# Kernel tuning notes

Measured on AMD Instinct MI355X. Metric: run time of the kernel, lower is better.

Reference implementation:

```python
import jax, jax.numpy as jnp
import numpy as np

# 22-joint tree (parents[i] < i); feet at 18, 21; spine at 2 (stand-in for get_totalcapture_skeleton)
PARENTS = [-1, 0, 1, 2, 3, 4, 3, 6, 7, 8, 3, 10, 11, 12, 1, 14, 15, 16, 17, 1, 19, 20]
FEET = [18, 21]
SPINE = 2
LAMBDAS = dict(root=5.0, rot=1.0, pos=2.0, vel=1.0, smooth=0.5, contact=2.0, floor=2.0, tilt=1.0)


def _normalize(x, eps=1e-12):
    return x / jnp.maximum(jnp.linalg.norm(x, axis=-1, keepdims=True), eps)


def cont6d_to_mat(d6):
    # d6: (..., 6) -> (..., 3, 3) with columns (b1, b2, b3)
    a1, a2 = d6[..., :3], d6[..., 3:]
    b1 = _normalize(a1)
    b2 = _normalize(a2 - b1 * jnp.sum(b1 * a2, axis=-1, keepdims=True))
    b3 = jnp.cross(b1, b2)
    return jnp.stack((b1, b2, b3), axis=-1)


def run_canonical_fk(full_output, offsets):
    # full_output: (B, S, 22, 6); root forced to identity rot / zero pos
    B, S, J, _ = full_output.shape
    rot_mats = cont6d_to_mat(full_output)  # (B, S, 22, 3, 3)
    eye = jnp.broadcast_to(jnp.eye(3, dtype=full_output.dtype), (B, S, 3, 3))
    zeros = jnp.zeros((B, S, 3), dtype=full_output.dtype)
    g_rots = [None] * J
    g_pos = [None] * J
    g_rots[0], g_pos[0] = eye, zeros
    for i in range(1, J):
        p = PARENTS[i]
        g_rots[i] = jnp.einsum('bsij,bsjk->bsik', g_rots[p], rot_mats[:, :, i])
        g_pos[i] = g_pos[p] + jnp.einsum('bsij,j->bsi', g_rots[p], offsets[i])
    return jnp.stack(g_pos, axis=2)  # (B, S, 22, 3)


def mse(a, b):
    return jnp.mean(jnp.square(a - b))


def motion_loss(pred_full, target_full, offsets):
    l_root = mse(pred_full[:, :, 0, :3], target_full[:, :, 0, :3]) + \
             mse(pred_full[:, :, 1, :], target_full[:, :, 1, :])
    l_rot = mse(pred_full[:, :, 2:], target_full[:, :, 2:])

    pred_pos = run_canonical_fk(pred_full, offsets)
    gt_pos = run_canonical_fk(target_full, offsets)
    l_pos = mse(pred_pos, gt_pos)

    pred_vel = pred_pos[:, 1:] - pred_pos[:, :-1]
    gt_vel = gt_pos[:, 1:] - gt_pos[:, :-1]
    l_vel = mse(pred_vel, gt_vel)

    pred_acc = pred_vel[:, 1:] - pred_vel[:, :-1]
    gt_acc = gt_vel[:, 1:] - gt_vel[:, :-1]
    l_smooth = mse(pred_acc, gt_acc)

    feet = jnp.array(FEET)
    l_floor = mse(pred_pos[:, :, feet, 1], gt_pos[:, :, feet, 1])

    gt_feet_vel = gt_vel[:, :, feet, :]
    pred_feet_vel = pred_vel[:, :, feet, :]
    is_planted = (jnp.linalg.norm(gt_feet_vel, axis=-1) < 0.005).astype(pred_full.dtype)
    l_contact = jnp.mean(jnp.linalg.norm(pred_feet_vel, axis=-1) * is_planted)

    pred_spine = cont6d_to_mat(pred_full[:, :, SPINE])
    gt_spine = cont6d_to_mat(target_full[:, :, SPINE])
    # R @ [0,1,0]^T == second column of R
    l_tilt = mse(pred_spine[..., :, 1], gt_spine[..., :, 1])

    total = (LAMBDAS['root'] * l_root + LAMBDAS['rot'] * l_rot + LAMBDAS['pos'] * l_pos +
             LAMBDAS['vel'] * l_vel + LAMBDAS['smooth'] * l_smooth + LAMBDAS['contact'] * l_contact +
             LAMBDAS['floor'] * l_floor + LAMBDAS['tilt'] * l_tilt)
    return total


def setup_inputs() -> dict:
    key = jax.random.key(0)
    k1, k2 = jax.random.split(key)
    B, S, J, C = 256, 512, 22, 6
    pred_full = jax.random.normal(k1, (B, S, J, C), dtype=jnp.float32)
    target_full = jax.random.normal(k2, (B, S, J, C), dtype=jnp.float32)
    rng = np.random.default_rng(42)
    off = rng.normal(size=(J, 3)).astype(np.float32) * 0.1
    off[0] = 0.0
    offsets = jnp.asarray(off)
    return {"pred_full": pred_full, "target_full": target_full, "offsets": offsets}


def reference(pred_full, target_full, offsets):
    return motion_loss(pred_full, target_full, offsets)
```

## Files before the change

### kernel.cpp

```cpp
#include <hip/hip_runtime.h>

namespace {

constexpr int kB = 256;
constexpr int kS = 512;
constexpr int CHUNK  = 62;
constexpr int NCHUNK = (kS + CHUNK - 1) / CHUNK;
constexpr int NSLOT  = 64;
constexpr int LDSF   = 2304;

constexpr float BSf   = 131072.f;
constexpr float K_R1  = 5.0f / (BSf * 3.f);
constexpr float K_R2  = 5.0f / (BSf * 6.f);
constexpr float K_ROT = 1.0f / (BSf * 120.f);
constexpr float K_POS = 2.0f / (BSf * 66.f);
constexpr float K_VEL = 1.0f / (256.f * 511.f * 66.f);
constexpr float K_SMO = 0.5f / (256.f * 510.f * 66.f);
constexpr float K_FLO = 2.0f / (BSf * 2.f);
constexpr float K_CON = 2.0f / (256.f * 511.f * 2.f);
constexpr float K_TIL = 1.0f / (BSf * 3.f);

__device__ __forceinline__ void cont6d(const float a[6], float R[3][3]) {
    float n1 = a[0]*a[0] + a[1]*a[1] + a[2]*a[2];
    float i1 = __frsqrt_rn(fmaxf(n1, 1e-24f));
    float b1x = a[0]*i1, b1y = a[1]*i1, b1z = a[2]*i1;
    float dp  = b1x*a[3] + b1y*a[4] + b1z*a[5];
    float ux = a[3] - b1x*dp, uy = a[4] - b1y*dp, uz = a[5] - b1z*dp;
    float n2 = ux*ux + uy*uy + uz*uz;
    float i2 = __frsqrt_rn(fmaxf(n2, 1e-24f));
    float b2x = ux*i2, b2y = uy*i2, b2z = uz*i2;
    R[0][0] = b1x; R[1][0] = b1y; R[2][0] = b1z;
    R[0][1] = b2x; R[1][1] = b2y; R[2][1] = b2z;
    R[0][2] = b1y*b2z - b1z*b2y;
    R[1][2] = b1z*b2x - b1x*b2z;
    R[2][2] = b1x*b2y - b1y*b2x;
}

template<int C2, int FB>
__device__ __forceinline__ void stage(const float* __restrict__ pred,
                                      const float* __restrict__ targ,
                                      size_t rowbase, int s0,
                                      float* __restrict__ ldsw, int lane) {
    constexpr int V = 64 * C2;
    constexpr int R = (2 * V) / 64;
    const float* pp_ = pred + rowbase * 132 + FB;
    const float* tp_ = targ + rowbase * 132 + FB;
    float2 st[18];
    #pragma unroll
    for (int r = 0; r < R; ++r) {
        int u = r * 64 + lane;
        int t2 = (u >= V) ? 1 : 0;
        int uu = u - t2 * V;
        int f = uu / C2;
        int c = uu - f * C2;
        int sf = s0 + f; sf = (sf < kS) ? sf : (kS - 1);
        const float* bp = t2 ? tp_ : pp_;
        st[r] = *reinterpret_cast<const float2*>(bp + (size_t)sf * 132 + 2 * c);
    }
    float2* l2 = reinterpret_cast<float2*>(ldsw);
    #pragma unroll
    for (int r = 0; r < R; ++r)
        l2[r * 64 + lane] = st[r];
}

__device__ __forceinline__ void read6f(const float2* __restrict__ b, int jj, float a[6]) {
    float2 x = b[jj*3], y = b[jj*3+1], z = b[jj*3+2];
    a[0]=x.x; a[1]=x.y; a[2]=y.x; a[3]=y.y; a[4]=z.x; a[5]=z.y;
}

template<bool NEED_R, bool SPINE_J, bool FOOT>
__device__ __forceinline__ void joint_step(
    const float aP[6], const float aT[6], const float* __restrict__ off,
    const float RpP[3][3], const float ppP[3], float RnP[3][3], float pnP[3],
    const float RpT[3][3], const float ppT[3], float RnT[3][3], float pnT[3],
    float wf, float wv, float wa, float& s)
{
    float dsum = 0.f;
    #pragma unroll
    for (int k = 0; k < 6; ++k) { float dd = aP[k] - aT[k]; dsum += dd*dd; }
    s += wf * (K_ROT * dsum);

    const float ox = off[0], oy = off[1], oz = off[2];
    #pragma unroll
    for (int r = 0; r < 3; ++r) {
        pnP[r] = ppP[r] + RpP[r][0]*ox + RpP[r][1]*oy + RpP[r][2]*oz;
        pnT[r] = ppT[r] + RpT[r][0]*ox + RpT[r][1]*oy + RpT[r][2]*oz;
    }

    if constexpr (NEED_R) {
        float RlP[3][3], RlT[3][3];
        cont6d(aP, RlP);
        cont6d(aT, RlT);
        if constexpr (SPINE_J) {
            float t0 = RlP[0][1] - RlT[0][1];
            float t1 = RlP[1][1] - RlT[1][1];
            float t2 = RlP[2][1] - RlT[2][1];
            s += wf * (K_TIL * (t0*t0 + t1*t1 + t2*t2));
        }
        #pragma unroll
        for (int r = 0; r < 3; ++r)
            #pragma unroll
            for (int c = 0; c < 3; ++c) {
                RnP[r][c] = RpP[r][0]*RlP[0][c] + RpP[r][1]*RlP[1][c] + RpP[r][2]*RlP[2][c];
                RnT[r][c] = RpT[r][0]*RlT[0][c] + RpT[r][1]*RlT[1][c] + RpT[r][2]*RlT[2][c];
            }
    }

    float d[3], d1[3];
    #pragma unroll
    for (int r = 0; r < 3; ++r) d[r] = pnP[r] - pnT[r];
    s += wf * (K_POS * (d[0]*d[0] + d[1]*d[1] + d[2]*d[2]));

    float va = 0.f, sa = 0.f;
    #pragma unroll
    for (int r = 0; r < 3; ++r) {
        d1[r]    = __shfl_down(d[r], 1);
        float d2 = __shfl_down(d[r], 2);
        float dv = d1[r] - d[r];            va += dv*dv;
        float ds = d2 - 2.f*d1[r] + d[r];   sa += ds*ds;
    }
    s += wv * (K_VEL * va);
    s += wa * (K_SMO * sa);

    if constexpr (FOOT) {
        s += wf * (K_FLO * (d[1]*d[1]));
        float gx = __shfl_down(pnT[0], 1) - pnT[0];
        float gy = __shfl_down(pnT[1], 1) - pnT[1];
        float gz = __shfl_down(pnT[2], 1) - pnT[2];
        float pvx = gx + (d1[0] - d[0]);
        float pvy = gy + (d1[1] - d[1]);
        float pvz = gz + (d1[2] - d[2]);
        float planted = (gx*gx + gy*gy + gz*gz < 2.5e-5f) ? 1.f : 0.f;
        s += wv * (K_CON * (planted * sqrtf(pvx*pvx + pvy*pvy + pvz*pvz)));
    }
}

__global__ __launch_bounds__(64)
void motion_loss_kernel(const float* __restrict__ pred,
                        const float* __restrict__ targ,
                        const float* __restrict__ offs,
                        float* __restrict__ acc)
{
    __shared__ float lds[LDSF];

    const int lane = threadIdx.x;
    const int cg    = blockIdx.x;
    const int b     = cg / NCHUNK;
    const int chunk = cg - b * NCHUNK;
    const int s0    = chunk * CHUNK;
    const int s     = s0 + lane;
    const size_t rowbase = (size_t)b * kS;

    const float wf = (lane < CHUNK && s     < kS) ? 1.f : 0.f;
    const float wv = (lane < CHUNK && s + 1 < kS) ? 1.f : 0.f;
    const float wa = (lane < CHUNK && s + 2 < kS) ? 1.f : 0.f;

    float2* l2 = reinterpret_cast<float2*>(lds);
    const float2* pb9 = l2 + lane * 9;
    const float2* tb9 = l2 + 576 + lane * 9;

    float loss = 0.f;

    float R1P[3][3], R3P[3][3], RAP[3][3], RBP[3][3];
    float R1T[3][3], R3T[3][3], RAT[3][3], RBT[3][3];
    float p1[3], p3P[3], pAP[3], pBP[3], pSP[3];
    float          p3T[3], pAT[3], pBT[3], pST[3];
    auto& p1P = p1; auto& p1T = p1;

    #define JS(J, JJ, NR, SP, FT, RP, PP, RN, PN) { \
        float aP_[6], aT_[6]; read6f(pb9, JJ, aP_); read6f(tb9, JJ, aT_); \
        joint_step<NR, SP, FT>(aP_, aT_, offs + (J)*3, \
            RP##P, PP##P, RN##P, PN##P, RP##T, PP##T, RN##T, PN##T, \
            wf, wv, wa, loss); }
    #define SB __builtin_amdgcn_sched_barrier(0)

    stage<9, 0>(pred, targ, rowbase, s0, lds, lane);
    {
        float aP_[6], aT_[6];
        read6f(pb9, 0, aP_); read6f(tb9, 0, aT_);
        float d0 = aP_[0]-aT_[0], d1 = aP_[1]-aT_[1], d2 = aP_[2]-aT_[2];
        loss += wf * (K_R1 * (d0*d0 + d1*d1 + d2*d2));
    }
    {
        float aP_[6], aT_[6];
        read6f(pb9, 1, aP_); read6f(tb9, 1, aT_);
        float dsum = 0.f;
        #pragma unroll
        for (int k = 0; k < 6; ++k) { float dd = aP_[k]-aT_[k]; dsum += dd*dd; }
        loss += wf * (K_R2 * dsum);
        cont6d(aP_, R1P);
        cont6d(aT_, R1T);
        p1[0] = offs[3]; p1[1] = offs[4]; p1[2] = offs[5];
    }
    JS( 2, 2, true , true , false, R1, p1, RA, pA);

    SB; stage<9, 18>(pred, targ, rowbase, s0, lds, lane);
    JS( 3, 0, true , false, false, RA, pA, R3, p3);
    JS( 4, 1, true , false, false, R3, p3, RA, pA);
    JS( 5, 2, false, false, false, RA, pA, RB, pS);

    SB; stage<9, 36>(pred, targ, rowbase, s0, lds, lane);
    JS( 6, 0, true , false, false, R3, p3, RA, pA);
    JS( 7, 1, true , false, false, RA, pA, RB, pB);
    JS( 8, 2, true , false, false, RB, pB, RA, pA);

    SB; stage<9, 54>(pred, targ, rowbase, s0, lds, lane);
    JS( 9, 0, false, false, false, RA, pA, RB, pS);
    JS(10, 1, true , false, false, R3, p3, RB, pB);
    JS(11, 2, true , false, false, RB, pB, RA, pA);

    SB; stage<9, 72>(pred, targ, rowbase, s0, lds, lane);
    JS(12, 0, true , false, false, RA, pA, RB, pB);
    JS(13, 1, false, false, false, RB, pB, RA, pS);
    JS(14, 2, true , false, false, R1, p1, RA, pA);

    SB; stage<9, 90>(pred, targ, rowbase, s0, lds, lane);
    JS(15, 0, true , false, false, RA, pA, RB, pB);
    JS(16, 1, true , false, false, RB, pB, RA, pA);
    JS(17, 2, true , false, false, RA, pA, RB, pB);

    SB; stage<9, 108>(pred, targ, rowbase, s0, lds, lane);
    JS(18, 0, false, false, true , RB, pB, RA, pS);
    JS(19, 1, true , false, false, R1, p1, RA, pA);
    JS(20, 2, true , false, false, RA, pA, RB, pB);

    SB; stage<3, 126>(pred, targ, rowbase, s0, lds, lane);
    {
        const float2* pb3 = l2 + lane * 3;
        const float2* tb3 = l2 + 192 + lane * 3;
        float aP_[6], aT_[6];
        read6f(pb3, 0, aP_); read6f(tb3, 0, aT_);
        joint_step<false, false, true>(aP_, aT_, offs + 21*3,
            RBP, pBP, RAP, pSP, RBT, pBT, RAT, pST, wf, wv, wa, loss);
    }
    #undef JS
    #undef SB

    float v = loss;
    #pragma unroll
    for (int o = 32; o > 0; o >>= 1) v += __shfl_xor(v, o);
    if (lane == 0) atomicAdd(&acc[cg & (NSLOT - 1)], v);
}

__global__ void finalize_kernel(const float* __restrict__ acc, float* __restrict__ out) {
    float v = acc[threadIdx.x];
    #pragma unroll
    for (int o = 32; o > 0; o >>= 1) v += __shfl_xor(v, o);
    if (threadIdx.x == 0) out[0] = v;
}

}

extern "C" void kernel_launch(void* const* d_in, const int* in_sizes, int n_in,
                              void* d_out, int out_size, void* d_ws, size_t ws_size,
                              hipStream_t stream) {
    const float* pred = (const float*)d_in[0];
    const float* targ = (const float*)d_in[1];
    const float* offs = (const float*)d_in[2];
    float* acc = (float*)d_ws;

    hipMemsetAsync(acc, 0, NSLOT * sizeof(float), stream);
    motion_loss_kernel<<<dim3(kB * NCHUNK), dim3(64), 0, stream>>>(pred, targ, offs, acc);
    finalize_kernel<<<1, 64, 0, stream>>>(acc, (float*)d_out);
}
```

Before: 64.71 us.

## Triple-buffer global-to-LDS async loads with two joints per stage

Replaces the synchronous register-staged global-to-LDS copies with direct global_load_lds 16-byte asynchronous transfers into three rotating LDS buffers. Each stage now holds two joints (12 floats) for pred and target, and loads for later stages are issued ahead while the current joints are processed, with explicit vmcnt/lgkmcnt waits. This is meant to hide global memory latency behind the FK math in a single-wave block. It raises LDS use and depends on hand-counted wait values and on the single-wave LDS ordering being correct.

New measurement: 62.62 us. -3.2%, faster.

```diff
diff --git a/kernel.cpp b/kernel.cpp
--- a/kernel.cpp
+++ b/kernel.cpp
@@ -5,9 +5,10 @@
 constexpr int kB = 256;
 constexpr int kS = 512;
 constexpr int CHUNK  = 62;
-constexpr int NCHUNK = (kS + CHUNK - 1) / CHUNK;
+constexpr int NCHUNK = 9;
 constexpr int NSLOT  = 64;
-constexpr int LDSF   = 2304;
+constexpr int BUFF   = 1536;
+constexpr int LDSF   = 3 * BUFF;
 
 constexpr float BSf   = 131072.f;
 constexpr float K_R1  = 5.0f / (BSf * 3.f);
@@ -36,38 +37,6 @@
     R[2][2] = b1x*b2y - b1y*b2x;
 }
 
-template<int C2, int FB>
-__device__ __forceinline__ void stage(const float* __restrict__ pred,
-                                      const float* __restrict__ targ,
-                                      size_t rowbase, int s0,
-                                      float* __restrict__ ldsw, int lane) {
-    constexpr int V = 64 * C2;
-    constexpr int R = (2 * V) / 64;
-    const float* pp_ = pred + rowbase * 132 + FB;
-    const float* tp_ = targ + rowbase * 132 + FB;
-    float2 st[18];
-    #pragma unroll
-    for (int r = 0; r < R; ++r) {
-        int u = r * 64 + lane;
-        int t2 = (u >= V) ? 1 : 0;
-        int uu = u - t2 * V;
-        int f = uu / C2;
-        int c = uu - f * C2;
-        int sf = s0 + f; sf = (sf < kS) ? sf : (kS - 1);
-        const float* bp = t2 ? tp_ : pp_;
-        st[r] = *reinterpret_cast<const float2*>(bp + (size_t)sf * 132 + 2 * c);
-    }
-    float2* l2 = reinterpret_cast<float2*>(ldsw);
-    #pragma unroll
-    for (int r = 0; r < R; ++r)
-        l2[r * 64 + lane] = st[r];
-}
-
-__device__ __forceinline__ void read6f(const float2* __restrict__ b, int jj, float a[6]) {
-    float2 x = b[jj*3], y = b[jj*3+1], z = b[jj*3+2];
-    a[0]=x.x; a[1]=x.y; a[2]=y.x; a[3]=y.y; a[4]=z.x; a[5]=z.y;
-}
-
 template<bool NEED_R, bool SPINE_J, bool FOOT>
 __device__ __forceinline__ void joint_step(
     const float aP[6], const float aT[6], const float* __restrict__ off,
@@ -149,92 +118,155 @@
     const int chunk = cg - b * NCHUNK;
     const int s0    = chunk * CHUNK;
     const int s     = s0 + lane;
-    const size_t rowbase = (size_t)b * kS;
 
     const float wf = (lane < CHUNK && s     < kS) ? 1.f : 0.f;
     const float wv = (lane < CHUNK && s + 1 < kS) ? 1.f : 0.f;
     const float wa = (lane < CHUNK && s + 2 < kS) ? 1.f : 0.f;
 
-    float2* l2 = reinterpret_cast<float2*>(lds);
-    const float2* pb9 = l2 + lane * 9;
-    const float2* tb9 = l2 + 576 + lane * 9;
+    const float* predb = pred + (size_t)b * kS * 132;
+    const float* targb = targ + (size_t)b * kS * 132;
+
+    auto issue = [&](int FB, float* buf) {
+        #pragma unroll
+        for (int r = 0; r < 6; ++r) {
+            const float* tb = (r < 3) ? predb : targb;
+            int uu = (r % 3) * 64 + lane;
+            int f  = uu / 3;
+            int c  = uu - f * 3;
+            int sf = s0 + f; sf = (sf < kS) ? sf : (kS - 1);
+            const float* src = tb + (size_t)sf * 132 + FB + 4 * c;
+            __builtin_amdgcn_global_load_lds(
+                (const __attribute__((address_space(1))) void*)src,
+                (__attribute__((address_space(3))) void*)(buf + r * 256),
+                16, 0, 0);
+        }
+    };
+
+    float* buf0 = lds;
+    float* buf1 = lds + BUFF;
+    float* buf2 = lds + 2 * BUFF;
+
+    #define VW(N) do { asm volatile("s_waitcnt vmcnt(" #N ")" ::: "memory"); \
+                       __builtin_amdgcn_sched_barrier(0); } while (0)
+    #define LW0   do { asm volatile("s_waitcnt lgkmcnt(0)" ::: "memory"); \
+                       __builtin_amdgcn_sched_barrier(0); } while (0)
+
+    auto rd6 = [&](const float* base, int jj, float a[6]) {
+        const float2* q = reinterpret_cast<const float2*>(base + jj * 6);
+        float2 x = q[0], y = q[1], z = q[2];
+        a[0]=x.x; a[1]=x.y; a[2]=y.x; a[3]=y.y; a[4]=z.x; a[5]=z.y;
+    };
+
+    issue(0,  buf0);
+    issue(12, buf1);
+    issue(24, buf2);
 
     float loss = 0.f;
-
     float R1P[3][3], R3P[3][3], RAP[3][3], RBP[3][3];
     float R1T[3][3], R3T[3][3], RAT[3][3], RBT[3][3];
     float p1[3], p3P[3], pAP[3], pBP[3], pSP[3];
     float          p3T[3], pAT[3], pBT[3], pST[3];
     auto& p1P = p1; auto& p1T = p1;
 
-    #define JS(J, JJ, NR, SP, FT, RP, PP, RN, PN) { \
-        float aP_[6], aT_[6]; read6f(pb9, JJ, aP_); read6f(tb9, JJ, aT_); \
-        joint_step<NR, SP, FT>(aP_, aT_, offs + (J)*3, \
+    #define RD2(BUF) float aP0[6], aT0[6], aP1[6], aT1[6]; { \
+        const float* pb_ = (BUF) + lane * 12; \
+        const float* tb_ = (BUF) + 768 + lane * 12; \
+        rd6(pb_, 0, aP0); rd6(tb_, 0, aT0); rd6(pb_, 1, aP1); rd6(tb_, 1, aT1); }
+
+    #define JS(AP, AT, J, NR, SP, FT, RP, PP, RN, PN) \
+        joint_step<NR, SP, FT>(AP, AT, offs + (J)*3, \
             RP##P, PP##P, RN##P, PN##P, RP##T, PP##T, RN##T, PN##T, \
-            wf, wv, wa, loss); }
-    #define SB __builtin_amdgcn_sched_barrier(0)
-
-    stage<9, 0>(pred, targ, rowbase, s0, lds, lane);
-    {
-        float aP_[6], aT_[6];
-        read6f(pb9, 0, aP_); read6f(tb9, 0, aT_);
-        float d0 = aP_[0]-aT_[0], d1 = aP_[1]-aT_[1], d2 = aP_[2]-aT_[2];
-        loss += wf * (K_R1 * (d0*d0 + d1*d1 + d2*d2));
-    }
-    {
-        float aP_[6], aT_[6];
-        read6f(pb9, 1, aP_); read6f(tb9, 1, aT_);
-        float dsum = 0.f;
-        #pragma unroll
-        for (int k = 0; k < 6; ++k) { float dd = aP_[k]-aT_[k]; dsum += dd*dd; }
-        loss += wf * (K_R2 * dsum);
-        cont6d(aP_, R1P);
-        cont6d(aT_, R1T);
-        p1[0] = offs[3]; p1[1] = offs[4]; p1[2] = offs[5];
-    }
-    JS( 2, 2, true , true , false, R1, p1, RA, pA);
-
-    SB; stage<9, 18>(pred, targ, rowbase, s0, lds, lane);
-    JS( 3, 0, true , false, false, RA, pA, R3, p3);
-    JS( 4, 1, true , false, false, R3, p3, RA, pA);
-    JS( 5, 2, false, false, false, RA, pA, RB, pS);
-
-    SB; stage<9, 36>(pred, targ, rowbase, s0, lds, lane);
-    JS( 6, 0, true , false, false, R3, p3, RA, pA);
-    JS( 7, 1, true , false, false, RA, pA, RB, pB);
-    JS( 8, 2, true , false, false, RB, pB, RA, pA);
-
-    SB; stage<9, 54>(pred, targ, rowbase, s0, lds, lane);
-    JS( 9, 0, false, false, false, RA, pA, RB, pS);
-    JS(10, 1, true , false, false, R3, p3, RB, pB);
-    JS(11, 2, true , false, false, RB, pB, RA, pA);
-
-    SB; stage<9, 72>(pred, targ, rowbase, s0, lds, lane);
-    JS(12, 0, true , false, false, RA, pA, RB, pB);
-    JS(13, 1, false, false, false, RB, pB, RA, pS);
-    JS(14, 2, true , false, false, R1, p1, RA, pA);
-
-    SB; stage<9, 90>(pred, targ, rowbase, s0, lds, lane);
-    JS(15, 0, true , false, false, RA, pA, RB, pB);
-    JS(16, 1, true , false, false, RB, pB, RA, pA);
-    JS(17, 2, true , false, false, RA, pA, RB, pB);
-
-    SB; stage<9, 108>(pred, targ, rowbase, s0, lds, lane);
-    JS(18, 0, false, false, true , RB, pB, RA, pS);
-    JS(19, 1, true , false, false, R1, p1, RA, pA);
-    JS(20, 2, true , false, false, RA, pA, RB, pB);
-
-    SB; stage<3, 126>(pred, targ, rowbase, s0, lds, lane);
-    {
-        const float2* pb3 = l2 + lane * 3;
-        const float2* tb3 = l2 + 192 + lane * 3;
-        float aP_[6], aT_[6];
-        read6f(pb3, 0, aP_); read6f(tb3, 0, aT_);
-        joint_step<false, false, true>(aP_, aT_, offs + 21*3,
-            RBP, pBP, RAP, pSP, RBT, pBT, RAT, pST, wf, wv, wa, loss);
+            wf, wv, wa, loss)
+
+    VW(12);
+    {
+        RD2(buf0);
+        LW0; issue(36, buf0);
+        {
+            float d0 = aP0[0]-aT0[0], d1 = aP0[1]-aT0[1], d2 = aP0[2]-aT0[2];
+            loss += wf * (K_R1 * (d0*d0 + d1*d1 + d2*d2));
+        }
+        {
+            float dsum = 0.f;
+            #pragma unroll
+            for (int k = 0; k < 6; ++k) { float dd = aP1[k]-aT1[k]; dsum += dd*dd; }
+            loss += wf * (K_R2 * dsum);
+            cont6d(aP1, R1P);
+            cont6d(aT1, R1T);
+            p1[0] = offs[3]; p1[1] = offs[4]; p1[2] = offs[5];
+        }
+    }
+    VW(12);
+    {
+        RD2(buf1);
+        LW0; issue(48, buf1);
+        JS(aP0, aT0,  2, true , true , false, R1, p1, RA, pA);
+        JS(aP1, aT1,  3, true , false, false, RA, pA, R3, p3);
+    }
+    VW(12);
+    {
+        RD2(buf2);
+        LW0; issue(60, buf2);
+        JS(aP0, aT0,  4, true , false, false, R3, p3, RA, pA);
+        JS(aP1, aT1,  5, false, false, false, RA, pA, RB, pS);
+    }
+    VW(12);
+    {
+        RD2(buf0);
+        LW0; issue(72, buf0);
+        JS(aP0, aT0,  6, true , false, false, R3, p3, RA, pA);
+        JS(aP1, aT1,  7, true , false, false, RA, pA, RB, pB);
+    }
+    VW(12);
+    {
+        RD2(buf1);
+        LW0; issue(84, buf1);
+        JS(aP0, aT0,  8, true , false, false, RB, pB, RA, pA);
+        JS(aP1, aT1,  9, false, false, false, RA, pA, RB, pS);
+    }
+    VW(12);
+    {
+        RD2(buf2);
+        LW0; issue(96, buf2);
+        JS(aP0, aT0, 10, true , false, false, R3, p3, RB, pB);
+        JS(aP1, aT1, 11, true , false, false, RB, pB, RA, pA);
+    }
+    VW(12);
+    {
+        RD2(buf0);
+        LW0; issue(108, buf0);
+        JS(aP0, aT0, 12, true , false, false, RA, pA, RB, pB);
+        JS(aP1, aT1, 13, false, false, false, RB, pB, RA, pS);
+    }
+    VW(12);
+    {
+        RD2(buf1);
+        LW0; issue(120, buf1);
+        JS(aP0, aT0, 14, true , false, false, R1, p1, RA, pA);
+        JS(aP1, aT1, 15, true , false, false, RA, pA, RB, pB);
+    }
+    VW(12);
+    {
+        RD2(buf2);
+        JS(aP0, aT0, 16, true , false, false, RB, pB, RA, pA);
+        JS(aP1, aT1, 17, true , false, false, RA, pA, RB, pB);
+    }
+    VW(6);
+    {
+        RD2(buf0);
+        JS(aP0, aT0, 18, false, false, true , RB, pB, RA, pS);
+        JS(aP1, aT1, 19, true , false, false, R1, p1, RA, pA);
+    }
+    VW(0);
+    {
+        RD2(buf1);
+        JS(aP0, aT0, 20, true , false, false, RA, pA, RB, pB);
+        JS(aP1, aT1, 21, false, false, true , RB, pB, RA, pS);
     }
     #undef JS
-    #undef SB
+    #undef RD2
+    #undef VW
+    #undef LW0
 
     float v = loss;
     #pragma unroll
```
